# Optimization experiments

Hardware: AMD Instinct MI355X
Metric: run time of the kernel (lower is better)

The kernel has to match this reference:

```python
import jax, jax.numpy as jnp
import numpy as np

N_NODES = 100000
N_HYPEREDGES = 30000
N_INC = 300000
IN_CH = 128
HID = 256
OUT_CH = 128
EPS = 1e-5


def setup_inputs() -> dict:
    key = jax.random.key(0)
    ks = jax.random.split(key, 14)
    x = jax.random.normal(ks[0], (N_NODES, IN_CH), jnp.float32)
    node_idx = jax.random.randint(ks[1], (N_INC,), 0, N_NODES)
    he_idx = jax.random.randint(ks[2], (N_INC,), 0, N_HYPEREDGES)
    edge = jnp.stack([node_idx, he_idx], axis=0)  # [2, N_INC]
    s1 = 1.0 / np.sqrt(IN_CH)
    s2 = 1.0 / np.sqrt(HID)
    return {
        "x": x,
        "edge": edge,
        "W1": jax.random.normal(ks[3], (IN_CH, HID), jnp.float32) * s1,
        "b1": jnp.zeros((HID,), jnp.float32),
        "g1": jnp.ones((HID,), jnp.float32),
        "be1": jnp.zeros((HID,), jnp.float32),
        "W2": jax.random.normal(ks[4], (HID, HID), jnp.float32) * s2,
        "b2": jnp.zeros((HID,), jnp.float32),
        "g2": jnp.ones((HID,), jnp.float32),
        "be2": jnp.zeros((HID,), jnp.float32),
        "W3": jax.random.normal(ks[5], (HID, OUT_CH), jnp.float32) * s2,
        "b3": jnp.zeros((OUT_CH,), jnp.float32),
    }


def _hconv(x, node_idx, he_idx, W, b):
    # PyG HypergraphConv (no attention, unit hyperedge weights):
    # X' = D^{-1} H B^{-1} H^T (X @ W) + b
    x = x @ W  # [N, F]
    ones = jnp.ones((node_idx.shape[0],), x.dtype)
    d = jax.ops.segment_sum(ones, node_idx, num_segments=N_NODES)       # node degree
    bd = jax.ops.segment_sum(ones, he_idx, num_segments=N_HYPEREDGES)  # hyperedge degree
    Dinv = jnp.where(d > 0, 1.0 / jnp.maximum(d, 1.0), 0.0)
    Binv = jnp.where(bd > 0, 1.0 / jnp.maximum(bd, 1.0), 0.0)
    # node -> hyperedge aggregation, scaled by B^{-1}
    he = jax.ops.segment_sum(x[node_idx], he_idx, num_segments=N_HYPEREDGES) * Binv[:, None]
    # hyperedge -> node aggregation, scaled by D^{-1}
    out = jax.ops.segment_sum(he[he_idx], node_idx, num_segments=N_NODES) * Dinv[:, None]
    return out + b


def _bn(x, g, be):
    # BatchNorm1d, training mode (batch statistics over nodes)
    m = x.mean(axis=0)
    v = x.var(axis=0)
    return (x - m) * jax.lax.rsqrt(v + EPS) * g + be


def reference(x, edge, W1, b1, g1, be1, W2, b2, g2, be2, W3, b3):
    node_idx = edge[0]
    he_idx = edge[1]
    h = _bn(jax.nn.relu(_hconv(x, node_idx, he_idx, W1, b1)), g1, be1)
    h = _bn(jax.nn.relu(_hconv(h, node_idx, he_idx, W2, b2)), g2, be2)
    h = jax.nn.relu(_hconv(h, node_idx, he_idx, W3, b3))
    return h
```

## Files before the change

### kernel.cpp

```cpp
#include <hip/hip_runtime.h>

#define N_NODES 100000
#define N_HE    30000
#define N_INC   300000
#define HEPAD   30080
#define NREP    16

typedef short  short8  __attribute__((ext_vector_type(8)));
typedef float  floatx4 __attribute__((ext_vector_type(4)));
typedef unsigned int uintx4 __attribute__((ext_vector_type(4)));

__device__ inline unsigned short f2bf(float f) {
  unsigned int u = __float_as_uint(f);
  u = (u + 0x7fff + ((u >> 16) & 1)) >> 16;
  return (unsigned short)u;
}
__device__ inline unsigned int pack2(float lo, float hi) {
  return (unsigned int)f2bf(lo) | ((unsigned int)f2bf(hi) << 16);
}
__device__ inline void acc8(uint4 rv, float* a) {
  unsigned int u;
  u = rv.x; a[0] += __uint_as_float(u << 16); a[1] += __uint_as_float(u & 0xffff0000u);
  u = rv.y; a[2] += __uint_as_float(u << 16); a[3] += __uint_as_float(u & 0xffff0000u);
  u = rv.z; a[4] += __uint_as_float(u << 16); a[5] += __uint_as_float(u & 0xffff0000u);
  u = rv.w; a[6] += __uint_as_float(u << 16); a[7] += __uint_as_float(u & 0xffff0000u);
}

struct R4 { uint4 r[4]; };
struct R8 { uint4 r[8]; };

__device__ inline void load4(const unsigned short* __restrict__ base, const int* e,
                             int F, int c0, R4& o) {
#pragma unroll
  for (int k = 0; k < 4; k++)
    o.r[k] = *(const uint4*)(base + (size_t)e[k] * F + c0);
}
__device__ inline void accm4(const R4& o, int d, float* a) {
  if (d > 0) acc8(o.r[0], a);
  if (d > 1) acc8(o.r[1], a);
  if (d > 2) acc8(o.r[2], a);
  if (d > 3) acc8(o.r[3], a);
}
__device__ inline void load8(const unsigned short* __restrict__ base, const int* e,
                             int F, int c0, R8& o) {
#pragma unroll
  for (int k = 0; k < 8; k++)
    o.r[k] = *(const uint4*)(base + (size_t)e[k] * F + c0);
}
__device__ inline void accm8(const R8& o, int d, float* a) {
  acc8(o.r[0], a);
  if (d > 1) acc8(o.r[1], a);
  if (d > 2) acc8(o.r[2], a);
  if (d > 3) acc8(o.r[3], a);
  if (d > 4) acc8(o.r[4], a);
  if (d > 5) acc8(o.r[5], a);
  if (d > 6) acc8(o.r[6], a);
  if (d > 7) acc8(o.r[7], a);
}

__device__ inline void gather8p(const unsigned short* __restrict__ base,
                                const int* __restrict__ idx, int beg, int end,
                                int F, int c0, float* a) {
  if (beg >= end) return;
  int e[8];
#pragma unroll
  for (int k = 0; k < 8; k++) e[k] = idx[min(beg + k, end - 1)];
  for (int j = beg; j < end; j += 8) {
    R8 r;
    load8(base, e, F, c0, r);
    int jn = j + 8;
    if (jn < end) {
#pragma unroll
      for (int k = 0; k < 8; k++) e[k] = idx[min(jn + k, end - 1)];
    }
    __builtin_amdgcn_sched_barrier(0);
    accm8(r, end - j, a);
  }
}


__global__ void count_kernel(const int* __restrict__ nidx, const int* __restrict__ hidx,
                             int* __restrict__ node_cnt, int* __restrict__ he_cnt) {
  int i = blockIdx.x * blockDim.x + threadIdx.x;
  if (i < N_INC) {
    atomicAdd(&node_cnt[nidx[i]], 1);
    atomicAdd(&he_cnt[hidx[i]], 1);
  }
}

__global__ void scan1(const int* __restrict__ cnt, int* __restrict__ incl,
                      int* __restrict__ bsums, int n) {
  __shared__ int tmp[1024];
  int tid = threadIdx.x;
  int i = blockIdx.x * 1024 + tid;
  tmp[tid] = (i < n) ? cnt[i] : 0;
  __syncthreads();
  for (int off = 1; off < 1024; off <<= 1) {
    int t = (tid >= off) ? tmp[tid - off] : 0;
    __syncthreads();
    tmp[tid] += t;
    __syncthreads();
  }
  if (i < n) incl[i] = tmp[tid];
  if (tid == 1023) bsums[blockIdx.x] = tmp[1023];
}

__global__ void scan2(int* __restrict__ bsums, int nb) {
  __shared__ int tmp[128];
  int t = threadIdx.x;
  int my = (t < nb) ? bsums[t] : 0;
  tmp[t] = my;
  __syncthreads();
  for (int off = 1; off < 128; off <<= 1) {
    int v = (t >= off) ? tmp[t - off] : 0;
    __syncthreads();
    tmp[t] += v;
    __syncthreads();
  }
  if (t < nb) bsums[t] = tmp[t] - my;
}

__global__ void scan3(const int* __restrict__ cnt, const int* __restrict__ incl,
                      const int* __restrict__ bsums, int* __restrict__ ptr,
                      int* __restrict__ fill, int n) {
  int i = blockIdx.x * 1024 + threadIdx.x;
  if (i < n) {
    int e = incl[i] - cnt[i] + bsums[blockIdx.x];
    ptr[i] = e;
    fill[i] = e;
    if (i == n - 1) ptr[n] = incl[i] + bsums[blockIdx.x];
  }
}

__global__ void fill_kernel(const int* __restrict__ nidx, const int* __restrict__ hidx,
                            int* __restrict__ node_fill, int* __restrict__ he_fill,
                            int* __restrict__ node_hes, int* __restrict__ he_nodes) {
  int i = blockIdx.x * blockDim.x + threadIdx.x;
  if (i < N_INC) {
    int nn = nidx[i], hh = hidx[i];
    int p1 = atomicAdd(&node_fill[nn], 1);
    node_hes[p1] = hh;
    int p2 = atomicAdd(&he_fill[hh], 1);
    he_nodes[p2] = nn;
  }
}


__global__ void convert_x(const float* __restrict__ x, unsigned short* __restrict__ xb) {
  int i = blockIdx.x * 256 + threadIdx.x;
  if (i >= N_NODES * 16) return;
  const float4* p = (const float4*)x + (size_t)i * 2;
  float4 a = p[0], b = p[1];
  uint4 o;
  o.x = pack2(a.x, a.y); o.y = pack2(a.z, a.w);
  o.z = pack2(b.x, b.y); o.w = pack2(b.z, b.w);
  *(uint4*)(xb + (size_t)i * 8) = o;
}

__global__ __launch_bounds__(256) void fold_w(
    const float* __restrict__ W, const float* __restrict__ gsum,
    const float* __restrict__ gss, const float* __restrict__ g,
    const float* __restrict__ be, unsigned short* __restrict__ WT,
    float* __restrict__ cvec, int K, int N, float invN) {
  int n = blockIdx.y * 256 + threadIdx.x;
  if (n >= N) return;
  int k0 = blockIdx.x * 16;
  float c = 0.f;
  unsigned short loc[16];
#pragma unroll
  for (int i = 0; i < 16; i++) {
    int k = k0 + i;
    float w = W[(size_t)k * N + n];
    float s = 1.f, t = 0.f;
    if (gsum) {
      float ms = 0.f, vs = 0.f;
#pragma unroll
      for (int r = 0; r < NREP; r++) { ms += gsum[r * 256 + k]; vs += gss[r * 256 + k]; }
      float m = ms * invN;
      float v = vs * invN - m * m;
      s = g[k] * rsqrtf(v + 1e-5f);
      t = be[k] - m * s;
    }
    loc[i] = f2bf(w * s);
    c += t * w;
  }
  *(uint4*)(WT + (size_t)n * K + k0)     = *(const uint4*)&loc[0];
  *(uint4*)(WT + (size_t)n * K + k0 + 8) = *(const uint4*)&loc[8];
  atomicAdd(cvec + n, c);
}


__global__ __launch_bounds__(256) void gemm_mfma(
    const unsigned short* __restrict__ A, const unsigned short* __restrict__ BT,
    unsigned short* __restrict__ C, int K, int N) {
  __shared__ unsigned short As[128 * 32];
  __shared__ unsigned short Bs[128 * 32];
  const int tid  = threadIdx.x;
  const int w    = tid >> 6, lane = tid & 63;
  const int wm   = w & 1,  wn   = w >> 1;
  const int bm   = blockIdx.x * 128, bn = blockIdx.y * 128;
  const int quad = lane >> 4, r16 = lane & 15;

  floatx4 acc[4][4] = {};

  const int srow = (lane >> 2);
  const int scol = (lane & 3) * 8;

  for (int kb = 0; kb < K; kb += 32) {
#pragma unroll
    for (int i = 0; i < 2; i++) {
      const int row = (w * 2 + i) * 16 + srow;
      const unsigned short* ga = A  + (size_t)(bm + row) * K + kb + scol;
      const unsigned short* gb = BT + (size_t)(bn + row) * K + kb + scol;
      __builtin_amdgcn_global_load_lds(
          (const __attribute__((address_space(1))) void*)ga,
          (__attribute__((address_space(3))) void*)(&As[(w * 2 + i) * 512]), 16, 0, 0);
      __builtin_amdgcn_global_load_lds(
          (const __attribute__((address_space(1))) void*)gb,
          (__attribute__((address_space(3))) void*)(&Bs[(w * 2 + i) * 512]), 16, 0, 0);
    }
    __syncthreads();
    short8 af[4], bfr[4];
#pragma unroll
    for (int t = 0; t < 4; t++) {
      af[t]  = *(const short8*)&As[(wm * 64 + t * 16 + r16) * 32 + quad * 8];
      bfr[t] = *(const short8*)&Bs[(wn * 64 + t * 16 + r16) * 32 + quad * 8];
    }
#pragma unroll
    for (int mi = 0; mi < 4; mi++)
#pragma unroll
      for (int ni = 0; ni < 4; ni++)
        acc[mi][ni] = __builtin_amdgcn_mfma_f32_16x16x32_bf16(af[mi], bfr[ni], acc[mi][ni], 0, 0, 0);
    __syncthreads();
  }
#pragma unroll
  for (int mi = 0; mi < 4; mi++)
#pragma unroll
    for (int ni = 0; ni < 4; ni++)
#pragma unroll
      for (int rr = 0; rr < 4; rr++) {
        int gm = bm + wm * 64 + mi * 16 + quad * 4 + rr;
        int gn = bn + wn * 64 + ni * 16 + r16;
        C[(size_t)gm * N + gn] = f2bf(acc[mi][ni][rr]);
      }
}


__global__ __launch_bounds__(256, 4) void agg_he(
    const unsigned short* __restrict__ src, const int* __restrict__ ptr,
    const int* __restrict__ idx, unsigned short* __restrict__ dst,
    int F, int shift, int nSeg) {
  int seg = blockIdx.x * (256 >> shift) + (threadIdx.x >> shift);
  if (seg >= nSeg) return;
  int l = threadIdx.x & ((1 << shift) - 1);
  int c0 = l * 8;
  int beg = ptr[seg], end = ptr[seg + 1];
  float a[8] = {};
  gather8p(src, idx, beg, end, F, c0, a);
  float inv = (end > beg) ? 1.0f / (float)(end - beg) : 0.0f;
  uint4 o;
  o.x = pack2(a[0] * inv, a[1] * inv);
  o.y = pack2(a[2] * inv, a[3] * inv);
  o.z = pack2(a[4] * inv, a[5] * inv);
  o.w = pack2(a[6] * inv, a[7] * inv);
  *(uint4*)(dst + (size_t)seg * F + c0) = o;
}

__global__ __launch_bounds__(256, 4) void node_agg_bn(
    const unsigned short* __restrict__ he, const int* __restrict__ nptr,
    const int* __restrict__ nhes, const float* __restrict__ b,
    const float* __restrict__ cvec, unsigned short* __restrict__ dst,
    float* __restrict__ gsum, float* __restrict__ gss) {
  const int F = 256;
  const int bid = blockIdx.x;
  const int qi = (bid & 7) >> 1;
  const int xb = (bid >> 3) * 2 + (bid & 1);
  const int grp = threadIdx.x >> 3;
  const int l   = threadIdx.x & 7;
  const int c0  = qi * 64 + l * 8;
  float bb[8], cc[8];
#pragma unroll
  for (int j = 0; j < 8; j++) { bb[j] = b[c0 + j]; cc[j] = cvec[c0 + j]; }
  const int base_n = xb * 128 + grp * 4;
  int begs[4], ends[4];
#pragma unroll
  for (int i = 0; i < 4; i++) {
    int n = base_n + i;
    begs[i] = (n < N_NODES) ? nptr[n] : 0;
    ends[i] = (n < N_NODES) ? nptr[n + 1] : 0;
  }
  int e[4][4];
#pragma unroll
  for (int i = 0; i < 4; i++) {
#pragma unroll
    for (int k = 0; k < 4; k++)
      e[i][k] = (begs[i] < ends[i]) ? nhes[min(begs[i] + k, ends[i] - 1)] : 0;
  }
  R4 r0, r1, r2, r3;
  load4(he, e[0], F, c0, r0);
  load4(he, e[1], F, c0, r1);
  load4(he, e[2], F, c0, r2);
  load4(he, e[3], F, c0, r3);
  __builtin_amdgcn_sched_barrier(0);
  float sb[8] = {}, ssb[8] = {};
#pragma unroll
  for (int t = 0; t < 4; t++) {
    const int d = ends[t] - begs[t];
    float a[8] = {};
    const R4& rr = (t == 0) ? r0 : (t == 1) ? r1 : (t == 2) ? r2 : r3;
    accm4(rr, d, a);
    for (int j = begs[t] + 4; j < ends[t]; j += 4) {
      int et[4];
#pragma unroll
      for (int k = 0; k < 4; k++) et[k] = nhes[min(j + k, ends[t] - 1)];
      R4 tt; load4(he, et, F, c0, tt);
      accm4(tt, ends[t] - j, a);
    }
    const int n = base_n + t;
    if (n < N_NODES) {
      float inv  = (d > 0) ? 1.0f / (float)d : 0.0f;
      float cmul = (d > 0) ? 1.0f : 0.0f;
      float o[8];
#pragma unroll
      for (int j = 0; j < 8; j++) {
        o[j] = fmaxf(fmaf(a[j], inv, bb[j] + cmul * cc[j]), 0.f);
        sb[j] += o[j]; ssb[j] += o[j] * o[j];
      }
      uintx4 ov;
      ov.x = pack2(o[0], o[1]); ov.y = pack2(o[2], o[3]);
      ov.z = pack2(o[4], o[5]); ov.w = pack2(o[6], o[7]);
      __builtin_nontemporal_store(ov, (uintx4*)(dst + (size_t)n * F + c0));
    }
  }
  __shared__ float Ls[32][64];
  __shared__ float Lss[32][64];
#pragma unroll
  for (int j = 0; j < 8; j++) { Ls[grp][l * 8 + j] = sb[j]; Lss[grp][l * 8 + j] = ssb[j]; }
  __syncthreads();
  if (threadIdx.x < 64) {
    int c = threadIdx.x;
    float a1 = 0.f, a2 = 0.f;
#pragma unroll
    for (int h = 0; h < 32; h++) { a1 += Ls[h][c]; a2 += Lss[h][c]; }
    const int rep = xb & (NREP - 1);
    atomicAdd(gsum + rep * 256 + qi * 64 + c, a1);
    atomicAdd(gss  + rep * 256 + qi * 64 + c, a2);
  }
}

__global__ __launch_bounds__(256, 4) void agg_out(
    const unsigned short* __restrict__ he, const int* __restrict__ nptr,
    const int* __restrict__ nhes, const float* __restrict__ b,
    const float* __restrict__ cvec, float* __restrict__ out) {
  const int F = 128;
  const int bid = blockIdx.x;
  const int hi = (bid & 7) >> 2;
  const int xb = (bid >> 3) * 4 + (bid & 3);
  const int grp = threadIdx.x >> 3;
  const int l   = threadIdx.x & 7;
  const int c0  = hi * 64 + l * 8;
  float bb[8], cc[8];
#pragma unroll
  for (int j = 0; j < 8; j++) { bb[j] = b[c0 + j]; cc[j] = cvec[c0 + j]; }
  const int base_n = xb * 128 + grp * 4;
  int begs[4], ends[4];
#pragma unroll
  for (int i = 0; i < 4; i++) {
    int n = base_n + i;
    begs[i] = (n < N_NODES) ? nptr[n] : 0;
    ends[i] = (n < N_NODES) ? nptr[n + 1] : 0;
  }
  int e[4][4];
#pragma unroll
  for (int i = 0; i < 4; i++) {
#pragma unroll
    for (int k = 0; k < 4; k++)
      e[i][k] = (begs[i] < ends[i]) ? nhes[min(begs[i] + k, ends[i] - 1)] : 0;
  }
  R4 r0, r1, r2, r3;
  load4(he, e[0], F, c0, r0);
  load4(he, e[1], F, c0, r1);
  load4(he, e[2], F, c0, r2);
  load4(he, e[3], F, c0, r3);
  __builtin_amdgcn_sched_barrier(0);
#pragma unroll
  for (int t = 0; t < 4; t++) {
    const int d = ends[t] - begs[t];
    float a[8] = {};
    const R4& rr = (t == 0) ? r0 : (t == 1) ? r1 : (t == 2) ? r2 : r3;
    accm4(rr, d, a);
    for (int j = begs[t] + 4; j < ends[t]; j += 4) {
      int et[4];
#pragma unroll
      for (int k = 0; k < 4; k++) et[k] = nhes[min(j + k, ends[t] - 1)];
      R4 tt; load4(he, et, F, c0, tt);
      accm4(tt, ends[t] - j, a);
    }
    const int n = base_n + t;
    if (n < N_NODES) {
      float inv  = (d > 0) ? 1.0f / (float)d : 0.0f;
      float cmul = (d > 0) ? 1.0f : 0.0f;
      floatx4 o0, o1;
#pragma unroll
      for (int j = 0; j < 4; j++)
        o0[j] = fmaxf(fmaf(a[j], inv, bb[j] + cmul * cc[j]), 0.f);
#pragma unroll
      for (int j = 0; j < 4; j++)
        o1[j] = fmaxf(fmaf(a[4 + j], inv, bb[4 + j] + cmul * cc[4 + j]), 0.f);
      float* dp = out + (size_t)n * F + c0;
      __builtin_nontemporal_store(o0, (floatx4*)dp);
      __builtin_nontemporal_store(o1, (floatx4*)(dp + 4));
    }
  }
}


extern "C" void kernel_launch(void* const* d_in, const int* in_sizes, int n_in,
                              void* d_out, int out_size, void* d_ws, size_t ws_size,
                              hipStream_t stream) {
  const float* x    = (const float*)d_in[0];
  const int*   edge = (const int*)d_in[1];
  const int*   nidx = edge;
  const int*   hidx = edge + N_INC;
  const float* W1  = (const float*)d_in[2];
  const float* b1  = (const float*)d_in[3];
  const float* g1  = (const float*)d_in[4];
  const float* be1 = (const float*)d_in[5];
  const float* W2  = (const float*)d_in[6];
  const float* b2  = (const float*)d_in[7];
  const float* g2  = (const float*)d_in[8];
  const float* be2 = (const float*)d_in[9];
  const float* W3  = (const float*)d_in[10];
  const float* b3  = (const float*)d_in[11];
  float* out = (float*)d_out;

  char* ws = (char*)d_ws;
  size_t off = 0;
  auto alloc = [&](size_t bytes) -> void* {
    void* p = ws + off;
    off = (off + bytes + 255) & ~(size_t)255;
    return p;
  };
  unsigned short* Xb   = (unsigned short*)alloc((size_t)N_NODES * 128 * 2);
  unsigned short* Bb   = (unsigned short*)alloc((size_t)N_NODES * 256 * 2);
  unsigned short* Hraw = (unsigned short*)alloc((size_t)HEPAD * 256 * 2);
  unsigned short* HEb  = (unsigned short*)alloc((size_t)HEPAD * 256 * 2);
  unsigned short* W1T  = (unsigned short*)alloc((size_t)256 * 128 * 2);
  unsigned short* W2T  = (unsigned short*)alloc((size_t)256 * 256 * 2);
  unsigned short* W3T  = (unsigned short*)alloc((size_t)128 * 256 * 2);
  size_t zero_begin = off;
  int* he_cnt   = (int*)alloc((size_t)N_HE * 4);
  int* node_cnt = (int*)alloc((size_t)N_NODES * 4);
  float* gsum1 = (float*)alloc((size_t)NREP * 256 * 4);
  float* gss1  = (float*)alloc((size_t)NREP * 256 * 4);
  float* gsum2 = (float*)alloc((size_t)NREP * 256 * 4);
  float* gss2  = (float*)alloc((size_t)NREP * 256 * 4);
  float* c1 = (float*)alloc(1024);
  float* c2 = (float*)alloc(1024);
  float* c3 = (float*)alloc(1024);
  size_t zero_end = off;
  int* he_ptr    = (int*)alloc((size_t)(N_HE + 1) * 4);
  int* node_ptr  = (int*)alloc((size_t)(N_NODES + 1) * 4);
  int* he_fill   = (int*)alloc((size_t)N_HE * 4);
  int* node_fill = (int*)alloc((size_t)N_NODES * 4);
  int* he_nodes  = (int*)alloc((size_t)N_INC * 4);
  int* node_hes  = (int*)alloc((size_t)N_INC * 4);
  int* incl      = (int*)alloc((size_t)N_NODES * 4);
  int* bsums     = (int*)alloc(512);

  hipMemsetAsync((void*)(ws + zero_begin), 0, zero_end - zero_begin, stream);

  count_kernel<<<(N_INC + 255) / 256, 256, 0, stream>>>(nidx, hidx, node_cnt, he_cnt);
  {
    int nb = (N_HE + 1023) / 1024;
    scan1<<<nb, 1024, 0, stream>>>(he_cnt, incl, bsums, N_HE);
    scan2<<<1, 128, 0, stream>>>(bsums, nb);
    scan3<<<nb, 1024, 0, stream>>>(he_cnt, incl, bsums, he_ptr, he_fill, N_HE);
  }
  {
    int nb = (N_NODES + 1023) / 1024;
    scan1<<<nb, 1024, 0, stream>>>(node_cnt, incl, bsums, N_NODES);
    scan2<<<1, 128, 0, stream>>>(bsums, nb);
    scan3<<<nb, 1024, 0, stream>>>(node_cnt, incl, bsums, node_ptr, node_fill, N_NODES);
  }
  fill_kernel<<<(N_INC + 255) / 256, 256, 0, stream>>>(nidx, hidx, node_fill, he_fill,
                                                       node_hes, he_nodes);

  convert_x<<<(N_NODES * 16 + 255) / 256, 256, 0, stream>>>(x, Xb);
  { dim3 g(128 / 16, 1);
    fold_w<<<g, 256, 0, stream>>>(W1, nullptr, nullptr, nullptr, nullptr, W1T, c1, 128, 256, 0.f); }

  const int MBHE = HEPAD / 128;
  const int QB = (N_NODES + 127) / 128;
  const int GRID_NA = 8 * ((QB + 1) / 2);
  const int GRID_AO = 8 * ((QB + 3) / 4);
  const float invN = 1.0f / (float)N_NODES;

  agg_he<<<(N_HE + 15) / 16, 256, 0, stream>>>(Xb, he_ptr, he_nodes, Hraw, 128, 4, N_HE);
  { dim3 g(MBHE, 2); gemm_mfma<<<g, 256, 0, stream>>>(Hraw, W1T, HEb, 128, 256); }
  node_agg_bn<<<GRID_NA, 256, 0, stream>>>(HEb, node_ptr, node_hes, b1, c1,
                                           Bb, gsum1, gss1);

  { dim3 g(256 / 16, 1);
    fold_w<<<g, 256, 0, stream>>>(W2, gsum1, gss1, g1, be1, W2T, c2, 256, 256, invN); }
  agg_he<<<(N_HE + 7) / 8, 256, 0, stream>>>(Bb, he_ptr, he_nodes, Hraw, 256, 5, N_HE);
  { dim3 g(MBHE, 2); gemm_mfma<<<g, 256, 0, stream>>>(Hraw, W2T, HEb, 256, 256); }
  node_agg_bn<<<GRID_NA, 256, 0, stream>>>(HEb, node_ptr, node_hes, b2, c2,
                                           Bb, gsum2, gss2);

  { dim3 g(256 / 16, 1);
    fold_w<<<g, 256, 0, stream>>>(W3, gsum2, gss2, g2, be2, W3T, c3, 256, 128, invN); }
  agg_he<<<(N_HE + 7) / 8, 256, 0, stream>>>(Bb, he_ptr, he_nodes, Hraw, 256, 5, N_HE);
  { dim3 g(MBHE, 1); gemm_mfma<<<g, 256, 0, stream>>>(Hraw, W3T, HEb, 256, 128); }
  agg_out<<<GRID_AO, 256, 0, stream>>>(HEb, node_ptr, node_hes, b3, c3, out);
}
```

Measured before the change: 415.6 us.

## Store node features in column-sliced layout for cache-local hyperedge gathers

Node feature buffers (converted X and the BN outputs) are now written in a sliced layout: 16-column slices, each holding all nodes contiguously. The hyperedge aggregation kernel processes one slice per block group, so each gather touches a 3.2 MB slice that can stay cache-resident instead of striding over the full feature matrix. The producers now write scattered 16-byte chunks across slices, and the nontemporal store hint is dropped. The risk is less coalesced writes and more blocks doing redundant index reads per slice.

```diff
diff --git a/kernel.cpp b/kernel.cpp
--- a/kernel.cpp
+++ b/kernel.cpp
@@ -5,6 +5,7 @@
 #define N_INC   300000
 #define HEPAD   30080
 #define NREP    16
+#define SLICE_E (N_NODES * 16)
 
 typedef short  short8  __attribute__((ext_vector_type(8)));
 typedef float  floatx4 __attribute__((ext_vector_type(4)));
@@ -149,12 +150,14 @@
 __global__ void convert_x(const float* __restrict__ x, unsigned short* __restrict__ xb) {
   int i = blockIdx.x * 256 + threadIdx.x;
   if (i >= N_NODES * 16) return;
+  int n = i >> 4, cb = i & 15;
   const float4* p = (const float4*)x + (size_t)i * 2;
   float4 a = p[0], b = p[1];
   uint4 o;
   o.x = pack2(a.x, a.y); o.y = pack2(a.z, a.w);
   o.z = pack2(b.x, b.y); o.w = pack2(b.z, b.w);
-  *(uint4*)(xb + (size_t)i * 8) = o;
+  int si = cb >> 1, half = cb & 1;
+  *(uint4*)(xb + (size_t)si * SLICE_E + (size_t)n * 16 + half * 8) = o;
 }
 
 __global__ __launch_bounds__(256) void fold_w(
@@ -246,24 +249,29 @@
 }
 
 
-__global__ __launch_bounds__(256, 4) void agg_he(
+__global__ __launch_bounds__(256, 4) void agg_he_s(
     const unsigned short* __restrict__ src, const int* __restrict__ ptr,
     const int* __restrict__ idx, unsigned short* __restrict__ dst,
-    int F, int shift, int nSeg) {
-  int seg = blockIdx.x * (256 >> shift) + (threadIdx.x >> shift);
+    int Fd, int segb, int nSeg) {
+  const int bid = blockIdx.x;
+  const int g = bid >> 3;
+  const int phase = (g >= segb) ? 1 : 0;
+  const int si = (bid & 7) + 8 * phase;
+  const int sb = g - segb * phase;
+  const int seg = sb * 128 + (threadIdx.x >> 1);
   if (seg >= nSeg) return;
-  int l = threadIdx.x & ((1 << shift) - 1);
-  int c0 = l * 8;
+  const int l = threadIdx.x & 1;
+  const unsigned short* sbase = src + (size_t)si * SLICE_E + l * 8;
   int beg = ptr[seg], end = ptr[seg + 1];
   float a[8] = {};
-  gather8p(src, idx, beg, end, F, c0, a);
+  gather8p(sbase, idx, beg, end, 16, 0, a);
   float inv = (end > beg) ? 1.0f / (float)(end - beg) : 0.0f;
   uint4 o;
   o.x = pack2(a[0] * inv, a[1] * inv);
   o.y = pack2(a[2] * inv, a[3] * inv);
   o.z = pack2(a[4] * inv, a[5] * inv);
   o.w = pack2(a[6] * inv, a[7] * inv);
-  *(uint4*)(dst + (size_t)seg * F + c0) = o;
+  *(uint4*)(dst + (size_t)seg * Fd + si * 16 + l * 8) = o;
 }
 
 __global__ __launch_bounds__(256, 4) void node_agg_bn(
@@ -302,6 +310,8 @@
   load4(he, e[2], F, c0, r2);
   load4(he, e[3], F, c0, r3);
   __builtin_amdgcn_sched_barrier(0);
+  const int slice = c0 >> 4;
+  const int half  = l & 1;
   float sb[8] = {}, ssb[8] = {};
 #pragma unroll
   for (int t = 0; t < 4; t++) {
@@ -326,10 +336,10 @@
         o[j] = fmaxf(fmaf(a[j], inv, bb[j] + cmul * cc[j]), 0.f);
         sb[j] += o[j]; ssb[j] += o[j] * o[j];
       }
-      uintx4 ov;
+      uint4 ov;
       ov.x = pack2(o[0], o[1]); ov.y = pack2(o[2], o[3]);
       ov.z = pack2(o[4], o[5]); ov.w = pack2(o[6], o[7]);
-      __builtin_nontemporal_store(ov, (uintx4*)(dst + (size_t)n * F + c0));
+      *(uint4*)(dst + (size_t)slice * SLICE_E + (size_t)n * 16 + half * 8) = ov;
     }
   }
   __shared__ float Ls[32][64];
@@ -491,26 +501,27 @@
     fold_w<<<g, 256, 0, stream>>>(W1, nullptr, nullptr, nullptr, nullptr, W1T, c1, 128, 256, 0.f); }
 
   const int MBHE = HEPAD / 128;
+  const int SEGB = (N_HE + 127) / 128;
   const int QB = (N_NODES + 127) / 128;
   const int GRID_NA = 8 * ((QB + 1) / 2);
   const int GRID_AO = 8 * ((QB + 3) / 4);
   const float invN = 1.0f / (float)N_NODES;
 
-  agg_he<<<(N_HE + 15) / 16, 256, 0, stream>>>(Xb, he_ptr, he_nodes, Hraw, 128, 4, N_HE);
+  agg_he_s<<<8 * SEGB, 256, 0, stream>>>(Xb, he_ptr, he_nodes, Hraw, 128, SEGB, N_HE);
   { dim3 g(MBHE, 2); gemm_mfma<<<g, 256, 0, stream>>>(Hraw, W1T, HEb, 128, 256); }
   node_agg_bn<<<GRID_NA, 256, 0, stream>>>(HEb, node_ptr, node_hes, b1, c1,
                                            Bb, gsum1, gss1);
 
   { dim3 g(256 / 16, 1);
     fold_w<<<g, 256, 0, stream>>>(W2, gsum1, gss1, g1, be1, W2T, c2, 256, 256, invN); }
-  agg_he<<<(N_HE + 7) / 8, 256, 0, stream>>>(Bb, he_ptr, he_nodes, Hraw, 256, 5, N_HE);
+  agg_he_s<<<16 * SEGB, 256, 0, stream>>>(Bb, he_ptr, he_nodes, Hraw, 256, SEGB, N_HE);
   { dim3 g(MBHE, 2); gemm_mfma<<<g, 256, 0, stream>>>(Hraw, W2T, HEb, 256, 256); }
   node_agg_bn<<<GRID_NA, 256, 0, stream>>>(HEb, node_ptr, node_hes, b2, c2,
                                            Bb, gsum2, gss2);
 
   { dim3 g(256 / 16, 1);
     fold_w<<<g, 256, 0, stream>>>(W3, gsum2, gss2, g2, be2, W3T, c3, 256, 128, invN); }
-  agg_he<<<(N_HE + 7) / 8, 256, 0, stream>>>(Bb, he_ptr, he_nodes, Hraw, 256, 5, N_HE);
+  agg_he_s<<<16 * SEGB, 256, 0, stream>>>(Bb, he_ptr, he_nodes, Hraw, 256, SEGB, N_HE);
   { dim3 g(MBHE, 1); gemm_mfma<<<g, 256, 0, stream>>>(Hraw, W3T, HEb, 256, 128); }
   agg_out<<<GRID_AO, 256, 0, stream>>>(HEb, node_ptr, node_hes, b3, c3, out);
 }
```

Result: slower. 468.1 us (+12.6%).
